# Performance work log

Hardware: AMD Instinct MI355X
Metric: run time of the kernel (lower is better)

## Reference

```python
import jax, jax.numpy as jnp
import numpy as np

ALPHA = 3.0      # sharpness in tanh(alpha * lin(x)) (HypergraphConstructor)
TOPK = 10        # scale_hyperedges: neighbors per node in similarity topk
NEG_SLOPE = 0.2  # LeakyReLU slope in HypergraphAttention


def setup_inputs() -> dict:
    key = jax.random.key(0)
    ks = jax.random.split(key, 8)
    B, L, N, F, D, E = 16, 64, 512, 64, 64, 40
    return {
        "x": jax.random.normal(ks[0], (B, L, N, F), jnp.float32),
        "idx": jnp.arange(N, dtype=jnp.int64) if jax.config.jax_enable_x64 else jnp.arange(N, dtype=jnp.int32),
        "emb1": 0.1 * jax.random.normal(ks[1], (N, E), jnp.float32),
        "lin1_w": jax.random.normal(ks[2], (E, E), jnp.float32) / np.float32(np.sqrt(E)),
        "lin1_b": jnp.zeros((E,), jnp.float32),
        "W_self": 0.1 * jax.random.normal(ks[3], (F, D), jnp.float32),
        "W_neigh": 0.1 * jax.random.normal(ks[4], (F, D), jnp.float32),
        "W_concat": 0.1 * jax.random.normal(ks[5], (2 * D, D), jnp.float32),
        "attention": 0.1 * jax.random.normal(ks[6], (2 * D, 1), jnp.float32),
    }


def build_incidence(idx, emb1, lin1_w, lin1_b):
    """HypergraphConstructor (similarity-topk branch). Returns H: (N_nodes, M_hyperedges)."""
    feats = jnp.tanh(ALPHA * (emb1[idx] @ lin1_w + lin1_b))        # (N, E)
    sim = feats @ feats.T                                          # (N, N)
    _, top = jax.lax.top_k(sim, TOPK)                              # (N, k) indices
    n = feats.shape[0]
    rows = jnp.arange(n)[:, None]
    H = jnp.zeros((n, n), feats.dtype).at[rows, top].set(1.0)      # row i = hyperedge from node i's neighbors
    return H.T                                                     # (N nodes, M hyperedges)


def hypergraph_attention(x, H, W_self, W_neigh, W_concat, attention):
    """Faithful HypergraphAttention.forward (eval mode: dropout is identity)."""
    x_self = jnp.einsum('blnf,fd->blnd', x, W_self)
    # aggregate nodes -> hyperedges: H.T[m,n] == H[n,m]
    he = jnp.einsum('nm,blnf->blmf', H, x)                          # (B, L, M, F)
    e_deg = jnp.maximum(H.sum(axis=0), 1.0)                        # (M,)
    he = he / e_deg[None, None, :, None]
    he = jnp.where(he >= 0, he, NEG_SLOPE * he)                    # LeakyReLU(0.2)
    # scatter hyperedges -> nodes
    x_neigh = jnp.einsum('nm,blmf->blnf', H, he)                   # (B, L, N, F)
    n_deg = jnp.maximum(H.sum(axis=1), 1.0)                        # (N,)
    x_neigh = x_neigh / n_deg[None, None, :, None]
    x_neigh = jnp.einsum('blnf,fd->blnd', x_neigh, W_neigh)
    x_cat = jnp.concatenate([x_self, x_neigh], axis=-1)            # (B, L, N, 2D)
    scores = jnp.squeeze(x_cat @ attention, axis=-1)               # (B, L, N)
    w = jax.nn.softmax(scores, axis=-1)                            # softmax over nodes
    return (x_cat * w[..., None]) @ W_concat                       # (B, L, N, D)


def reference(x, idx, emb1, lin1_w, lin1_b, W_self, W_neigh, W_concat, attention):
    H = build_incidence(idx, emb1, lin1_w, lin1_b)
    return hypergraph_attention(x, H, W_self, W_neigh, W_concat, attention)
```

## Files before the change

kernel.cpp:

```cpp
#include <hip/hip_runtime.h>

#define N_NODES 512
#define E_DIM   40
#define TOPK    10

typedef unsigned short u16;
typedef __attribute__((ext_vector_type(8))) short short8;
typedef __attribute__((ext_vector_type(4))) float f32x4;

__device__ __forceinline__ u16 f2bf(float f) {
    unsigned int b = __float_as_uint(f);
    b += 0x7fffu + ((b >> 16) & 1u);
    return (u16)(b >> 16);
}
__device__ __forceinline__ float bf2f(u16 u) {
    return __uint_as_float(((unsigned int)u) << 16);
}
__device__ __forceinline__ unsigned pk2(float a, float b) {
    return (unsigned)f2bf(a) | ((unsigned)f2bf(b) << 16);
}

__global__ void prep_kernel(const float* __restrict__ emb1,
                            const float* __restrict__ w,
                            const float* __restrict__ b,
                            float* __restrict__ feats,
                            const float* __restrict__ Ws, const float* __restrict__ Wn,
                            const float* __restrict__ Wc, const float* __restrict__ att,
                            u16* __restrict__ Wt, float* __restrict__ ap) {
    if (blockIdx.x < N_NODES) {
        int n = blockIdx.x, e = threadIdx.x;
        if (e >= E_DIM) return;
        const float* er = emb1 + n * E_DIM;
        float s = b[e];
        for (int k = 0; k < E_DIM; ++k) s += er[k] * w[k * E_DIM + e];
        feats[n * E_DIM + e] = tanhf(3.0f * s);
    } else {
        int f = blockIdx.x - N_NODES, d = threadIdx.x;
        float a = 0.f, bb = 0.f;
        for (int k = 0; k < 64; ++k) {
            a  += Ws[f * 64 + k] * Wc[k * 64 + d];
            bb += Wn[f * 64 + k] * Wc[(64 + k) * 64 + d];
        }
        Wt[d * 128 + f]      = f2bf(a);
        Wt[d * 128 + 64 + f] = f2bf(bb);
        float p0 = Ws[f * 64 + d] * att[d];
        float p1 = Wn[f * 64 + d] * att[64 + d];
        for (int off = 32; off > 0; off >>= 1) {
            p0 += __shfl_down(p0, off);
            p1 += __shfl_down(p1, off);
        }
        if (d == 0) { ap[f] = p0; ap[64 + f] = p1; }
    }
}

#define TOPK_SMEM (512 * 41 * 4 + 4 * 512 * 4)

__global__ __launch_bounds__(256) void topk_kernel(const float* __restrict__ feats,
                                                   u16* __restrict__ top16) {
    extern __shared__ float tsm[];
    float* sf   = tsm;
    float* ssim = tsm + 512 * 41;
    const int tid = threadIdx.x;
    for (int i = tid; i < 512 * E_DIM; i += 256) {
        int n = i / E_DIM, k = i - n * E_DIM;
        sf[n * 41 + k] = feats[i];
    }
    __syncthreads();
    const int wv = tid >> 6, lane = tid & 63;
    const int m = blockIdx.x * 4 + wv;
    float* sim = ssim + wv * 512;

    float fm[E_DIM];
#pragma unroll
    for (int k = 0; k < E_DIM; ++k) fm[k] = sf[m * 41 + k];
    for (int n = lane; n < N_NODES; n += 64) {
        const float* fr = &sf[n * 41];
        float s = 0.f;
#pragma unroll
        for (int k = 0; k < E_DIM; ++k) s += fm[k] * fr[k];
        sim[n] = s;
    }
    __syncthreads();
    for (int it = 0; it < TOPK; ++it) {
        float bv = -3.0e38f; int bi = 1 << 30;
        for (int n = lane; n < N_NODES; n += 64) {
            float v = sim[n];
            if (v > bv) { bv = v; bi = n; }
        }
        for (int off = 32; off > 0; off >>= 1) {
            float ov = __shfl_down(bv, off);
            int   oi = __shfl_down(bi, off);
            if (ov > bv || (ov == bv && oi < bi)) { bv = ov; bi = oi; }
        }
        bi = __shfl(bi, 0);
        if (lane == 0) top16[m * 16 + it] = (u16)bi;
        __syncthreads();
        sim[bi] = -3.0e38f;
        __syncthreads();
    }
}

__global__ void hbuild_kernel(const u16* __restrict__ top16,
                              u16* __restrict__ Hrow, u16* __restrict__ H,
                              int* __restrict__ deg) {
    int m = threadIdx.x;
#pragma unroll
    for (int j = 0; j < TOPK; ++j) {
        int n = (int)top16[m * 16 + j];
        Hrow[m * 512 + n] = 0x3F80;
        H[n * 512 + m]    = 0x3F80;
        atomicAdd(&deg[n], 1);
    }
}

#define R0_OFF 0
#define R1_OFF 65536
#define SC_OFF 131072
#define RED_OFF 133120
#define SMEM_BYTES 133184

__device__ __forceinline__ int rm_byte(int n, int g) {
    return n * 128 + ((g ^ (n & 7)) << 4);
}
__device__ __forceinline__ int t64_byte(int f, int g) {
    return f * 1024 + ((g ^ (f & 7)) << 4);
}

__global__ __launch_bounds__(512, 2) void main_kernel(
    const float* __restrict__ x,
    const u16* __restrict__ Hrow, const u16* __restrict__ H,
    const int* __restrict__ deg,
    const u16* __restrict__ Wt, const float* __restrict__ ap,
    float* __restrict__ out)
{
    extern __shared__ char smem[];
    float* sc  = (float*)(smem + SC_OFF);
    float* red = (float*)(smem + RED_OFF);

    const int bl  = blockIdx.x;
    const int tid = threadIdx.x;
    const int wv = tid >> 6, lane = tid & 63;
    const int lrow = lane & 15, lk = lane >> 4;
    const float* xr   = x   + (size_t)bl * N_NODES * 64;
    float*       outr = out + (size_t)bl * N_NODES * 64;

    float s = 0.f;
    {
        const float4* px = (const float4*)(xr + tid * 64);
#pragma unroll
        for (int g = 0; g < 8; ++g) {
            float4 v0 = px[2 * g], v1 = px[2 * g + 1];
            float4 a0 = *(const float4*)(ap + g * 8);
            float4 a1 = *(const float4*)(ap + g * 8 + 4);
            s += v0.x * a0.x + v0.y * a0.y + v0.z * a0.z + v0.w * a0.w
               + v1.x * a1.x + v1.y * a1.y + v1.z * a1.z + v1.w * a1.w;
            *(uint4*)(smem + R0_OFF + rm_byte(tid, g)) =
                make_uint4(pk2(v0.x, v0.y), pk2(v0.z, v0.w),
                           pk2(v1.x, v1.y), pk2(v1.z, v1.w));
        }
    }
    __syncthreads();

    {
        const int ng = tid >> 3, fg = tid & 7;
        uint4 R[8];
#pragma unroll
        for (int i = 0; i < 8; ++i)
            R[i] = *(const uint4*)(smem + R0_OFF + rm_byte(ng * 8 + i, fg));
#pragma unroll
        for (int j = 0; j < 8; ++j) {
            unsigned wds[4];
#pragma unroll
            for (int p = 0; p < 4; ++p) {
                unsigned lo = ((const unsigned*)&R[2 * p])[j >> 1];
                unsigned hi = ((const unsigned*)&R[2 * p + 1])[j >> 1];
                lo = (j & 1) ? (lo >> 16) : (lo & 0xffffu);
                hi = (j & 1) ? (hi >> 16) : (hi & 0xffffu);
                wds[p] = lo | (hi << 16);
            }
            *(uint4*)(smem + R1_OFF + t64_byte(fg * 8 + j, ng)) =
                make_uint4(wds[0], wds[1], wds[2], wds[3]);
        }
    }
    __syncthreads();

    {
        f32x4 acc[4][4];
#pragma unroll
        for (int mt = 0; mt < 4; ++mt)
#pragma unroll
            for (int ft = 0; ft < 4; ++ft) acc[mt][ft] = (f32x4)0.f;
        for (int ks = 0; ks < 16; ++ks) {
            short8 afr[4], bfr[4];
#pragma unroll
            for (int mt = 0; mt < 4; ++mt)
                afr[mt] = *(const short8*)(Hrow + (wv * 64 + mt * 16 + lrow) * 512
                                                + ks * 32 + lk * 8);
#pragma unroll
            for (int ft = 0; ft < 4; ++ft)
                bfr[ft] = *(const short8*)(smem + R1_OFF
                                         + t64_byte(ft * 16 + lrow, ks * 4 + lk));
#pragma unroll
            for (int mt = 0; mt < 4; ++mt)
#pragma unroll
                for (int ft = 0; ft < 4; ++ft)
                    acc[mt][ft] = __builtin_amdgcn_mfma_f32_16x16x32_bf16(
                        afr[mt], bfr[ft], acc[mt][ft], 0, 0, 0);
        }
#pragma unroll
        for (int mt = 0; mt < 4; ++mt) {
            const int gm = wv * 8 + mt * 2 + (lk >> 1);
#pragma unroll
            for (int ft = 0; ft < 4; ++ft) {
                const int f = ft * 16 + lrow;
                float v[4];
#pragma unroll
                for (int r = 0; r < 4; ++r) {
                    float t = acc[mt][ft][r] * 0.1f;
                    v[r] = t >= 0.f ? t : 0.2f * t;
                }
                uint2 pkv = make_uint2(pk2(v[0], v[1]), pk2(v[2], v[3]));
                *(uint2*)(smem + R0_OFF + t64_byte(f, gm) + (lk & 1) * 8) = pkv;
            }
        }
    }
    __syncthreads();

    {
        f32x4 acc[4][4];
#pragma unroll
        for (int nt = 0; nt < 4; ++nt)
#pragma unroll
            for (int ft = 0; ft < 4; ++ft) acc[nt][ft] = (f32x4)0.f;
        for (int ks = 0; ks < 16; ++ks) {
            short8 afr[4], bfr[4];
#pragma unroll
            for (int ft = 0; ft < 4; ++ft)
                afr[ft] = *(const short8*)(smem + R0_OFF
                                         + t64_byte(ft * 16 + lrow, ks * 4 + lk));
#pragma unroll
            for (int nt = 0; nt < 4; ++nt)
                bfr[nt] = *(const short8*)(H + (wv * 64 + nt * 16 + lrow) * 512
                                             + ks * 32 + lk * 8);
#pragma unroll
            for (int nt = 0; nt < 4; ++nt)
#pragma unroll
                for (int ft = 0; ft < 4; ++ft)
                    acc[nt][ft] = __builtin_amdgcn_mfma_f32_16x16x32_bf16(
                        afr[ft], bfr[nt], acc[nt][ft], 0, 0, 0);
        }
        __syncthreads();
#pragma unroll
        for (int nt = 0; nt < 4; ++nt) {
            const int n = wv * 64 + nt * 16 + lrow;
            int dg = deg[n];
            const float ideg = 1.0f / (float)(dg > 0 ? dg : 1);
#pragma unroll
            for (int ft = 0; ft < 4; ++ft) {
                const int gf = ft * 2 + (lk >> 1);
                uint2 pkv = make_uint2(pk2(acc[nt][ft][0] * ideg, acc[nt][ft][1] * ideg),
                                       pk2(acc[nt][ft][2] * ideg, acc[nt][ft][3] * ideg));
                *(uint2*)(smem + R1_OFF + rm_byte(n, gf) + (lk & 1) * 8) = pkv;
            }
        }
    }
    __syncthreads();

#pragma unroll
    for (int g = 0; g < 8; ++g) {
        short8 q = *(const short8*)(smem + R1_OFF + rm_byte(tid, g));
        float4 b0 = *(const float4*)(ap + 64 + g * 8);
        float4 b1 = *(const float4*)(ap + 64 + g * 8 + 4);
        s += bf2f((u16)q[0]) * b0.x + bf2f((u16)q[1]) * b0.y
           + bf2f((u16)q[2]) * b0.z + bf2f((u16)q[3]) * b0.w
           + bf2f((u16)q[4]) * b1.x + bf2f((u16)q[5]) * b1.y
           + bf2f((u16)q[6]) * b1.z + bf2f((u16)q[7]) * b1.w;
    }
    float bv = s;
#pragma unroll
    for (int off = 32; off > 0; off >>= 1) bv = fmaxf(bv, __shfl_xor(bv, off));
    if (lane == 0) red[wv] = bv;
    __syncthreads();
    float M = red[0];
#pragma unroll
    for (int w = 1; w < 8; ++w) M = fmaxf(M, red[w]);
    float ev = expf(s - M);
    sc[tid] = ev;
    float sv = ev;
#pragma unroll
    for (int off = 32; off > 0; off >>= 1) sv += __shfl_xor(sv, off);
    if (lane == 0) red[8 + wv] = sv;
    __syncthreads();
    float S = red[8];
#pragma unroll
    for (int w = 1; w < 8; ++w) S += red[8 + w];
    const float invS = 1.0f / S;

    {
        for (int nt = 0; nt < 4; ++nt) {
            const int n = wv * 64 + nt * 16 + lrow;
            f32x4 accn[4];
#pragma unroll
            for (int dt = 0; dt < 4; ++dt) accn[dt] = (f32x4)0.f;
#pragma unroll
            for (int ks = 0; ks < 4; ++ks) {
                short8 bfrag;
                if (ks < 2) {
                    const float4* px = (const float4*)(xr + n * 64 + ks * 32 + lk * 8);
                    float4 v0 = px[0], v1 = px[1];
                    union { uint4 u; short8 s8; } cv;
                    cv.u.x = pk2(v0.x, v0.y); cv.u.y = pk2(v0.z, v0.w);
                    cv.u.z = pk2(v1.x, v1.y); cv.u.w = pk2(v1.z, v1.w);
                    bfrag = cv.s8;
                } else {
                    int gx = (ks - 2) * 4 + lk;
                    bfrag = *(const short8*)(smem + R1_OFF + rm_byte(n, gx));
                }
#pragma unroll
                for (int dt = 0; dt < 4; ++dt) {
                    short8 wfrag = *(const short8*)(Wt + (dt * 16 + lrow) * 128
                                                       + ks * 32 + lk * 8);
                    accn[dt] = __builtin_amdgcn_mfma_f32_16x16x32_bf16(
                        wfrag, bfrag, accn[dt], 0, 0, 0);
                }
            }
            const float ww = sc[n] * invS;
#pragma unroll
            for (int dt = 0; dt < 4; ++dt) {
                float4 f;
                f.x = accn[dt][0] * ww; f.y = accn[dt][1] * ww;
                f.z = accn[dt][2] * ww; f.w = accn[dt][3] * ww;
                *(float4*)(outr + n * 64 + dt * 16 + lk * 4) = f;
            }
        }
    }
}

#define WS_FEATS 0
#define WS_TOP   81920
#define WS_WT    98304
#define WS_AP    114688
#define WS_DEG   115200
#define WS_HROW  131072
#define WS_H     655360
#define WS_END   1179648

extern "C" void kernel_launch(void* const* d_in, const int* in_sizes, int n_in,
                              void* d_out, int out_size, void* d_ws, size_t ws_size,
                              hipStream_t stream) {
    const float* x        = (const float*)d_in[0];
    const float* emb1     = (const float*)d_in[2];
    const float* lin1_w   = (const float*)d_in[3];
    const float* lin1_b   = (const float*)d_in[4];
    const float* W_self   = (const float*)d_in[5];
    const float* W_neigh  = (const float*)d_in[6];
    const float* W_concat = (const float*)d_in[7];
    const float* att      = (const float*)d_in[8];
    float* out = (float*)d_out;

    char* ws = (char*)d_ws;
    float* feats = (float*)(ws + WS_FEATS);
    u16*   top16 = (u16*)  (ws + WS_TOP);
    u16*   Wt    = (u16*)  (ws + WS_WT);
    float* ap    = (float*)(ws + WS_AP);
    int*   deg   = (int*)  (ws + WS_DEG);
    u16*   Hrow  = (u16*)  (ws + WS_HROW);
    u16*   H     = (u16*)  (ws + WS_H);

    prep_kernel<<<N_NODES + 64, 64, 0, stream>>>(emb1, lin1_w, lin1_b, feats,
                                                 W_self, W_neigh, W_concat, att, Wt, ap);

    (void)hipFuncSetAttribute((const void*)topk_kernel,
                              hipFuncAttributeMaxDynamicSharedMemorySize, TOPK_SMEM);
    topk_kernel<<<128, 256, TOPK_SMEM, stream>>>(feats, top16);

    (void)hipMemsetAsync(ws + WS_DEG, 0, WS_END - WS_DEG, stream);
    hbuild_kernel<<<1, 512, 0, stream>>>(top16, Hrow, H, deg);

    (void)hipFuncSetAttribute((const void*)main_kernel,
                              hipFuncAttributeMaxDynamicSharedMemorySize, SMEM_BYTES);
    main_kernel<<<1024, 512, SMEM_BYTES, stream>>>(x, Hrow, H, deg, Wt, ap, out);
}
```

Before: 271.0 us.

## Halve shared memory by single LDS buffer and direct transposed stores

Shrinks the main kernel's LDS footprint from two 64KB buffers to one. The row-major staging pass and the separate in-LDS transpose are replaced by writing each bf16 element of x straight into the transposed layout. A barrier is added so the buffer can be safely reused between stages. Launch bounds rise to four blocks per CU to take advantage of the lower LDS use. The trade-off is many scattered 2-byte LDS stores that may cause bank conflicts, plus added register pressure from the tighter launch bound.

```diff
diff --git a/kernel.cpp b/kernel.cpp
--- a/kernel.cpp
+++ b/kernel.cpp
@@ -113,11 +113,9 @@
     }
 }
 
-#define R0_OFF 0
-#define R1_OFF 65536
-#define SC_OFF 131072
-#define RED_OFF 133120
-#define SMEM_BYTES 133184
+#define SC_OFF  65536
+#define RED_OFF 67584
+#define SMEM_BYTES 67648
 
 __device__ __forceinline__ int rm_byte(int n, int g) {
     return n * 128 + ((g ^ (n & 7)) << 4);
@@ -126,7 +124,7 @@
     return f * 1024 + ((g ^ (f & 7)) << 4);
 }
 
-__global__ __launch_bounds__(512, 2) void main_kernel(
+__global__ __launch_bounds__(512, 4) void main_kernel(
     const float* __restrict__ x,
     const u16* __restrict__ Hrow, const u16* __restrict__ H,
     const int* __restrict__ deg,
@@ -147,6 +145,7 @@
     float s = 0.f;
     {
         const float4* px = (const float4*)(xr + tid * 64);
+        const int gcol = tid >> 3, bcol = (tid & 7) * 2;
 #pragma unroll
         for (int g = 0; g < 8; ++g) {
             float4 v0 = px[2 * g], v1 = px[2 * g + 1];
@@ -154,32 +153,12 @@
             float4 a1 = *(const float4*)(ap + g * 8 + 4);
             s += v0.x * a0.x + v0.y * a0.y + v0.z * a0.z + v0.w * a0.w
                + v1.x * a1.x + v1.y * a1.y + v1.z * a1.z + v1.w * a1.w;
-            *(uint4*)(smem + R0_OFF + rm_byte(tid, g)) =
-                make_uint4(pk2(v0.x, v0.y), pk2(v0.z, v0.w),
-                           pk2(v1.x, v1.y), pk2(v1.z, v1.w));
-        }
-    }
-    __syncthreads();
-
-    {
-        const int ng = tid >> 3, fg = tid & 7;
-        uint4 R[8];
-#pragma unroll
-        for (int i = 0; i < 8; ++i)
-            R[i] = *(const uint4*)(smem + R0_OFF + rm_byte(ng * 8 + i, fg));
-#pragma unroll
-        for (int j = 0; j < 8; ++j) {
-            unsigned wds[4];
-#pragma unroll
-            for (int p = 0; p < 4; ++p) {
-                unsigned lo = ((const unsigned*)&R[2 * p])[j >> 1];
-                unsigned hi = ((const unsigned*)&R[2 * p + 1])[j >> 1];
-                lo = (j & 1) ? (lo >> 16) : (lo & 0xffffu);
-                hi = (j & 1) ? (hi >> 16) : (hi & 0xffffu);
-                wds[p] = lo | (hi << 16);
-            }
-            *(uint4*)(smem + R1_OFF + t64_byte(fg * 8 + j, ng)) =
-                make_uint4(wds[0], wds[1], wds[2], wds[3]);
+            float vf[8] = { v0.x, v0.y, v0.z, v0.w, v1.x, v1.y, v1.z, v1.w };
+#pragma unroll
+            for (int j = 0; j < 8; ++j) {
+                int f = g * 8 + j;
+                *(u16*)(smem + t64_byte(f, gcol) + bcol) = f2bf(vf[j]);
+            }
         }
     }
     __syncthreads();
@@ -198,8 +177,7 @@
                                                 + ks * 32 + lk * 8);
 #pragma unroll
             for (int ft = 0; ft < 4; ++ft)
-                bfr[ft] = *(const short8*)(smem + R1_OFF
-                                         + t64_byte(ft * 16 + lrow, ks * 4 + lk));
+                bfr[ft] = *(const short8*)(smem + t64_byte(ft * 16 + lrow, ks * 4 + lk));
 #pragma unroll
             for (int mt = 0; mt < 4; ++mt)
 #pragma unroll
@@ -207,6 +185,7 @@
                     acc[mt][ft] = __builtin_amdgcn_mfma_f32_16x16x32_bf16(
                         afr[mt], bfr[ft], acc[mt][ft], 0, 0, 0);
         }
+        __syncthreads();
 #pragma unroll
         for (int mt = 0; mt < 4; ++mt) {
             const int gm = wv * 8 + mt * 2 + (lk >> 1);
@@ -219,8 +198,8 @@
                     float t = acc[mt][ft][r] * 0.1f;
                     v[r] = t >= 0.f ? t : 0.2f * t;
                 }
-                uint2 pkv = make_uint2(pk2(v[0], v[1]), pk2(v[2], v[3]));
-                *(uint2*)(smem + R0_OFF + t64_byte(f, gm) + (lk & 1) * 8) = pkv;
+                *(uint2*)(smem + t64_byte(f, gm) + (lk & 1) * 8) =
+                    make_uint2(pk2(v[0], v[1]), pk2(v[2], v[3]));
             }
         }
     }
@@ -236,8 +215,7 @@
             short8 afr[4], bfr[4];
 #pragma unroll
             for (int ft = 0; ft < 4; ++ft)
-                afr[ft] = *(const short8*)(smem + R0_OFF
-                                         + t64_byte(ft * 16 + lrow, ks * 4 + lk));
+                afr[ft] = *(const short8*)(smem + t64_byte(ft * 16 + lrow, ks * 4 + lk));
 #pragma unroll
             for (int nt = 0; nt < 4; ++nt)
                 bfr[nt] = *(const short8*)(H + (wv * 64 + nt * 16 + lrow) * 512
@@ -258,9 +236,9 @@
 #pragma unroll
             for (int ft = 0; ft < 4; ++ft) {
                 const int gf = ft * 2 + (lk >> 1);
-                uint2 pkv = make_uint2(pk2(acc[nt][ft][0] * ideg, acc[nt][ft][1] * ideg),
-                                       pk2(acc[nt][ft][2] * ideg, acc[nt][ft][3] * ideg));
-                *(uint2*)(smem + R1_OFF + rm_byte(n, gf) + (lk & 1) * 8) = pkv;
+                *(uint2*)(smem + rm_byte(n, gf) + (lk & 1) * 8) =
+                    make_uint2(pk2(acc[nt][ft][0] * ideg, acc[nt][ft][1] * ideg),
+                               pk2(acc[nt][ft][2] * ideg, acc[nt][ft][3] * ideg));
             }
         }
     }
@@ -268,7 +246,7 @@
 
 #pragma unroll
     for (int g = 0; g < 8; ++g) {
-        short8 q = *(const short8*)(smem + R1_OFF + rm_byte(tid, g));
+        short8 q = *(const short8*)(smem + rm_byte(tid, g));
         float4 b0 = *(const float4*)(ap + 64 + g * 8);
         float4 b1 = *(const float4*)(ap + 64 + g * 8 + 4);
         s += bf2f((u16)q[0]) * b0.x + bf2f((u16)q[1]) * b0.y
@@ -314,7 +292,7 @@
                     bfrag = cv.s8;
                 } else {
                     int gx = (ks - 2) * 4 + lk;
-                    bfrag = *(const short8*)(smem + R1_OFF + rm_byte(n, gx));
+                    bfrag = *(const short8*)(smem + rm_byte(n, gx));
                 }
 #pragma unroll
                 for (int dt = 0; dt < 4; ++dt) {
```

Result: faster. 243.7 us (-10.1%).
